# Optimization experiments

Hardware: AMD Instinct MI355X
Metric: run time of the kernel (lower is better)

The kernel has to match this reference:

```python
import jax, jax.numpy as jnp
import numpy as np

N_NODES = 100000


def _gcn_layer(x, W, b, row, col, norm, n_nodes):
    # x: [N, Fin], W: [Fin, Fout]. GCN: A_hat @ (x W) + b with symmetric norm.
    xw = x @ W                                   # [N, Fout]
    msg = xw[row] * norm[:, None]                # [E+N, Fout] gathered messages
    agg = jax.ops.segment_sum(msg, col, num_segments=n_nodes)  # scatter-add at dst
    return agg + b


def setup_inputs() -> dict:
    key = jax.random.key(0)
    ks = jax.random.split(key, 5)
    N, E = N_NODES, 1600000
    Fin, F1, F2, C = 512, 64, 128, 40
    x = jax.random.normal(ks[0], (N, Fin), dtype=jnp.float32)
    edge_index = jax.random.randint(ks[1], (2, E), 0, N, dtype=jnp.int64)
    W1 = jax.random.normal(ks[2], (Fin, F1), dtype=jnp.float32) / np.sqrt(Fin)
    W2 = jax.random.normal(ks[3], (F1, F2), dtype=jnp.float32) / np.sqrt(F1)
    W3 = jax.random.normal(ks[4], (F2, C), dtype=jnp.float32) / np.sqrt(F2)
    return {
        "x": x, "edge_index": edge_index,
        "W1": W1, "b1": jnp.zeros((F1,), jnp.float32),
        "W2": W2, "b2": jnp.zeros((F2,), jnp.float32),
        "W3": W3, "b3": jnp.zeros((C,), jnp.float32),
    }


def reference(x, edge_index, W1, b1, W2, b2, W3, b3):
    N = x.shape[0]
    # Add self-loops (GCNConv default add_self_loops=True)
    loop = jnp.arange(N, dtype=edge_index.dtype)
    row = jnp.concatenate([edge_index[0], loop])  # source nodes
    col = jnp.concatenate([edge_index[1], loop])  # destination nodes
    # Symmetric degree normalization: deg computed at destination with self-loops
    deg = jax.ops.segment_sum(jnp.ones_like(col, dtype=x.dtype), col, num_segments=N)
    dis = jax.lax.rsqrt(deg)                      # deg >= 1 due to self-loops
    norm = dis[row] * dis[col]                    # [E+N]

    h1 = jax.nn.relu(_gcn_layer(x, W1, b1, row, col, norm, N))
    # dropout is identity (training=False)
    h2 = jax.nn.relu(_gcn_layer(h1, W2, b2, row, col, norm, N))
    h3 = _gcn_layer(h2, W3, b3, row, col, norm, N)
    return jax.nn.log_softmax(h3, axis=1)
```

## Files before the change

kernel.cpp:

```cpp
#include <hip/hip_runtime.h>
#include <math.h>


typedef __attribute__((ext_vector_type(8))) short short8;
typedef __attribute__((ext_vector_type(4))) float f32x4;

__device__ __forceinline__ unsigned short f2bf(float f) {
    unsigned int u = __float_as_uint(f);
    unsigned int r = (u + 0x7fffu + ((u >> 16) & 1u)) >> 16;
    return (unsigned short)r;
}
__device__ __forceinline__ float bflo(unsigned int u) { return __uint_as_float(u << 16); }
__device__ __forceinline__ float bfhi(unsigned int u) { return __uint_as_float(u & 0xffff0000u); }

__device__ __forceinline__ void wprep_one(const float* W, unsigned short* out,
                                          int KS, int FOUT, int t) {
    int i = t & 7;
    int l = (t >> 3) & 63;
    int g = t >> 9;
    int ks = g % KS;
    int nt = g / KS;
    int k = ks * 32 + (l >> 4) * 8 + i;
    int c = nt * 16 + (l & 15);
    out[t] = (c < FOUT) ? f2bf(W[(size_t)k * FOUT + c]) : (unsigned short)0;
}

__global__ void prep_kernel(const float* __restrict__ W1, const float* __restrict__ W2,
                            const float* __restrict__ W3,
                            unsigned short* __restrict__ Wf1, unsigned short* __restrict__ Wf2,
                            unsigned short* __restrict__ Wf3,
                            int* __restrict__ cnt, int* __restrict__ fillc, int N) {
    int t = blockIdx.x * 256 + threadIdx.x;
    if (t < 32768)       wprep_one(W1, Wf1, 16, 64, t);
    else if (t < 40960)  wprep_one(W2, Wf2, 2, 128, t - 32768);
    else if (t < 47104)  wprep_one(W3, Wf3, 4, 40, t - 40960);
    if (t < N) cnt[t] = 0;
    else if (t < 2 * N) fillc[t - N] = 0;
}

__global__ void count_kernel(const int* __restrict__ col, int* __restrict__ cnt, int E) {
    int e = blockIdx.x * 256 + threadIdx.x;
    if (e < E) atomicAdd(&cnt[col[e]], 1);
}

__global__ void scan1_kernel(const int* __restrict__ cnt, int* __restrict__ out,
                             int* __restrict__ bsums, int n) {
    __shared__ int s[1024];
    int i = blockIdx.x * 1024 + threadIdx.x;
    int v = (i < n) ? cnt[i] : 0;
    s[threadIdx.x] = v;
    __syncthreads();
    for (int off = 1; off < 1024; off <<= 1) {
        int t = 0;
        if ((int)threadIdx.x >= off) t = s[threadIdx.x - off];
        __syncthreads();
        if ((int)threadIdx.x >= off) s[threadIdx.x] += t;
        __syncthreads();
    }
    if (i < n) out[i] = s[threadIdx.x] - v;
    if (threadIdx.x == 1023) bsums[blockIdx.x] = s[1023];
}

__global__ void scan2_kernel(int* bsums, int nb) {
    __shared__ int s[128];
    int v = ((int)threadIdx.x < nb) ? bsums[threadIdx.x] : 0;
    s[threadIdx.x] = v;
    __syncthreads();
    for (int off = 1; off < 128; off <<= 1) {
        int t = 0;
        if ((int)threadIdx.x >= off) t = s[threadIdx.x - off];
        __syncthreads();
        if ((int)threadIdx.x >= off) s[threadIdx.x] += t;
        __syncthreads();
    }
    if ((int)threadIdx.x < nb) bsums[threadIdx.x] = s[threadIdx.x] - v;
}

__global__ void scan3d_kernel(int* __restrict__ ptr, const int* __restrict__ bsums,
                              const int* __restrict__ cnt, float* __restrict__ dis,
                              int n, int E) {
    int i = blockIdx.x * 1024 + threadIdx.x;
    if (i < n) {
        ptr[i] += bsums[blockIdx.x];
        dis[i] = rsqrtf((float)(cnt[i] + 1));
    }
    if (i == 0) ptr[n] = E;
}

__global__ void fill_kernel(const int* __restrict__ row, const int* __restrict__ col,
                            const int* __restrict__ ptr, int* __restrict__ fillc,
                            const float* __restrict__ dis, uint2* __restrict__ csr_en, int E) {
    int e = blockIdx.x * 256 + threadIdx.x;
    if (e < E) {
        int c = col[e];
        int r = row[e];
        int p = ptr[c] + atomicAdd(&fillc[c], 1);
        uint2 en;
        en.x = (unsigned int)r;
        en.y = __float_as_uint(dis[r] * dis[c]);
        csr_en[p] = en;
    }
}

__global__ __launch_bounds__(256) void gemm1_kernel(const float* __restrict__ Ap,
                                                    const unsigned short* __restrict__ Wf,
                                                    unsigned short* __restrict__ Y, int N) {
    __shared__ unsigned short As[2][64][136];
    const int t = threadIdx.x;
    const int lane = t & 63;
    const int wid = t >> 6;
    const int rbase = blockIdx.x * 64;
    const int fr = lane & 15;
    const int khalf = lane >> 4;

    f32x4 acc[4];
#pragma unroll
    for (int nt = 0; nt < 4; nt++)
#pragma unroll
        for (int j = 0; j < 4; j++) acc[nt][j] = 0.f;

    auto stage = [&](int buf, int c) {
#pragma unroll
        for (int rd = 0; rd < 8; rd++) {
            int u = t + rd * 256;
            int row = u >> 5;
            int q = u & 31;
            int gr = rbase + row; if (gr > N - 1) gr = N - 1;
            float4 v = *(const float4*)(Ap + (size_t)gr * 512 + c * 128 + q * 4);
            uint2 w;
            w.x = (unsigned int)f2bf(v.x) | ((unsigned int)f2bf(v.y) << 16);
            w.y = (unsigned int)f2bf(v.z) | ((unsigned int)f2bf(v.w) << 16);
            *(uint2*)&As[buf][row][q * 4] = w;
        }
    };

    stage(0, 0);
    __syncthreads();
#pragma unroll
    for (int c = 0; c < 4; c++) {
        if (c < 3) stage((c + 1) & 1, c + 1);
#pragma unroll
        for (int ks = 0; ks < 4; ks++) {
            short8 afr = *(const short8*)&As[c & 1][wid * 16 + fr][ks * 32 + khalf * 8];
            const int ksg = c * 4 + ks;
#pragma unroll
            for (int nt = 0; nt < 4; nt++) {
                short8 bfr = *(const short8*)(Wf + (((size_t)nt * 16 + ksg) * 64 + lane) * 8);
                acc[nt] = __builtin_amdgcn_mfma_f32_16x16x32_bf16(afr, bfr, acc[nt], 0, 0, 0);
            }
        }
        __syncthreads();
    }

    const int rD0 = rbase + wid * 16 + (lane >> 4) * 4;
    const int colb = lane & 15;
#pragma unroll
    for (int nt = 0; nt < 4; nt++) {
        int c = nt * 16 + colb;
#pragma unroll
        for (int i = 0; i < 4; i++) {
            int rD = rD0 + i;
            if (rD < N) Y[(size_t)rD * 64 + c] = f2bf(acc[nt][i]);
        }
    }
}

__global__ __launch_bounds__(256) void gemm23_kernel(const unsigned short* __restrict__ A,
                                                     const unsigned short* __restrict__ Wf2,
                                                     const float* __restrict__ b2,
                                                     const unsigned short* __restrict__ Wf3,
                                                     unsigned short* __restrict__ Y, int N) {
    __shared__ unsigned short hs[4][16][136];
    const int lane = threadIdx.x & 63;
    const int wid = threadIdx.x >> 6;
    const int rbase = blockIdx.x * 64 + wid * 16;
    const int rA = rbase + (lane & 15);
    const bool va = rA < N;
    const int khalf = lane >> 4;

    f32x4 acc2[8];
#pragma unroll
    for (int nt = 0; nt < 8; nt++)
#pragma unroll
        for (int j = 0; j < 4; j++) acc2[nt][j] = 0.f;

#pragma unroll
    for (int ks = 0; ks < 2; ks++) {
        short8 afr;
        if (va) afr = *(const short8*)(A + (size_t)rA * 64 + ks * 32 + khalf * 8);
        else {
#pragma unroll
            for (int j = 0; j < 8; j++) afr[j] = 0;
        }
#pragma unroll
        for (int nt = 0; nt < 8; nt++) {
            short8 bfr = *(const short8*)(Wf2 + (((size_t)nt * 2 + ks) * 64 + lane) * 8);
            acc2[nt] = __builtin_amdgcn_mfma_f32_16x16x32_bf16(afr, bfr, acc2[nt], 0, 0, 0);
        }
    }

    const int rD = (lane >> 4) * 4;
    const int colb = lane & 15;
#pragma unroll
    for (int nt = 0; nt < 8; nt++) {
        int c = nt * 16 + colb;
        float bv = b2[c];
#pragma unroll
        for (int j = 0; j < 4; j++)
            hs[wid][rD + j][c] = f2bf(fmaxf(acc2[nt][j] + bv, 0.f));
    }
    __syncthreads();

    f32x4 acc3[3];
#pragma unroll
    for (int nt = 0; nt < 3; nt++)
#pragma unroll
        for (int j = 0; j < 4; j++) acc3[nt][j] = 0.f;

    const int r = lane & 15;
#pragma unroll
    for (int ks = 0; ks < 4; ks++) {
        short8 afr = *(const short8*)&hs[wid][r][ks * 32 + khalf * 8];
#pragma unroll
        for (int nt = 0; nt < 3; nt++) {
            short8 bfr = *(const short8*)(Wf3 + (((size_t)nt * 4 + ks) * 64 + lane) * 8);
            acc3[nt] = __builtin_amdgcn_mfma_f32_16x16x32_bf16(afr, bfr, acc3[nt], 0, 0, 0);
        }
    }

#pragma unroll
    for (int nt = 0; nt < 3; nt++) {
        int c = nt * 16 + colb;
        if (c < 40) {
#pragma unroll
            for (int i = 0; i < 4; i++) {
                int rr = rbase + rD + i;
                if (rr < N) Y[(size_t)rr * 40 + c] = f2bf(acc3[nt][i]);
            }
        }
    }
}

template <bool BR>
__global__ __launch_bounds__(256) void agg64_kernel(const unsigned int* __restrict__ XW,
                                                    const float* __restrict__ bias,
                                                    const int* __restrict__ ptr,
                                                    const uint2* __restrict__ EN,
                                                    unsigned int* __restrict__ Y, int N) {
    const int lane = threadIdx.x & 63;
    const int wid = threadIdx.x >> 6;
    const int n = blockIdx.x * 4 + wid;
    if (n >= N) return;
    const int s = lane >> 3;
    const int q = lane & 7;

    const int e0 = ptr[n], e1 = ptr[n + 1];
    const float selfw = 1.0f / (float)(e1 - e0 + 1);

    float acc[8];
    if (s == 0) {
        const uint4 u = *(const uint4*)(XW + (size_t)n * 32 + q * 4);
        acc[0] = selfw * bflo(u.x); acc[1] = selfw * bfhi(u.x);
        acc[2] = selfw * bflo(u.y); acc[3] = selfw * bfhi(u.y);
        acc[4] = selfw * bflo(u.z); acc[5] = selfw * bfhi(u.z);
        acc[6] = selfw * bflo(u.w); acc[7] = selfw * bfhi(u.w);
    } else {
#pragma unroll
        for (int j = 0; j < 8; j++) acc[j] = 0.f;
    }

    for (int eb = e0; eb < e1; eb += 64) {
        int cnt = e1 - eb; if (cnt > 64) cnt = 64;
        uint2 en;
        if (lane < cnt) en = EN[eb + lane];
        else { en.x = 0; en.y = 0; }
#pragma unroll 2
        for (int k = s; k < cnt; k += 8) {
            int r = __shfl((int)en.x, k);
            float nrm = __uint_as_float((unsigned int)__shfl((int)en.y, k));
            const uint4 u = *(const uint4*)(XW + (size_t)r * 32 + q * 4);
            acc[0] += nrm * bflo(u.x); acc[1] += nrm * bfhi(u.x);
            acc[2] += nrm * bflo(u.y); acc[3] += nrm * bfhi(u.y);
            acc[4] += nrm * bflo(u.z); acc[5] += nrm * bfhi(u.z);
            acc[6] += nrm * bflo(u.w); acc[7] += nrm * bfhi(u.w);
        }
    }

#pragma unroll
    for (int off = 8; off < 64; off <<= 1)
#pragma unroll
        for (int j = 0; j < 8; j++) acc[j] += __shfl_xor(acc[j], off);

    if (lane < 8) {
        float v[8];
        if (BR) {
            const float4 b0 = *((const float4*)bias + lane * 2);
            const float4 b1 = *((const float4*)bias + lane * 2 + 1);
            v[0] = fmaxf(acc[0] + b0.x, 0.f); v[1] = fmaxf(acc[1] + b0.y, 0.f);
            v[2] = fmaxf(acc[2] + b0.z, 0.f); v[3] = fmaxf(acc[3] + b0.w, 0.f);
            v[4] = fmaxf(acc[4] + b1.x, 0.f); v[5] = fmaxf(acc[5] + b1.y, 0.f);
            v[6] = fmaxf(acc[6] + b1.z, 0.f); v[7] = fmaxf(acc[7] + b1.w, 0.f);
        } else {
#pragma unroll
            for (int j = 0; j < 8; j++) v[j] = acc[j];
        }
        uint4 o;
        o.x = (unsigned int)f2bf(v[0]) | ((unsigned int)f2bf(v[1]) << 16);
        o.y = (unsigned int)f2bf(v[2]) | ((unsigned int)f2bf(v[3]) << 16);
        o.z = (unsigned int)f2bf(v[4]) | ((unsigned int)f2bf(v[5]) << 16);
        o.w = (unsigned int)f2bf(v[6]) | ((unsigned int)f2bf(v[7]) << 16);
        *(uint4*)(Y + (size_t)n * 32 + lane * 4) = o;
    }
}

__global__ __launch_bounds__(256) void agg40lsm_kernel(const unsigned int* __restrict__ XW,
                                                       const float* __restrict__ bias,
                                                       const int* __restrict__ ptr,
                                                       const uint2* __restrict__ EN,
                                                       float* __restrict__ out, int N) {
    const int lane = threadIdx.x & 63;
    const int wid = threadIdx.x >> 6;
    const int n = blockIdx.x * 4 + wid;
    if (n >= N) return;
    const int s = lane >> 4;
    const int c = lane & 15;
    const bool act = (c < 10);

    const int e0 = ptr[n], e1 = ptr[n + 1];
    const float selfw = 1.0f / (float)(e1 - e0 + 1);

    float acc[4] = {0.f, 0.f, 0.f, 0.f};
    if (s == 0 && act) {
        const uint2 u = *(const uint2*)(XW + (size_t)n * 20 + c * 2);
        acc[0] = selfw * bflo(u.x); acc[1] = selfw * bfhi(u.x);
        acc[2] = selfw * bflo(u.y); acc[3] = selfw * bfhi(u.y);
    }

    for (int eb = e0; eb < e1; eb += 64) {
        int cnt = e1 - eb; if (cnt > 64) cnt = 64;
        uint2 en;
        if (lane < cnt) en = EN[eb + lane];
        else { en.x = 0; en.y = 0; }
#pragma unroll 2
        for (int k = s; k < cnt; k += 4) {
            int r = __shfl((int)en.x, k);
            float nrm = __uint_as_float((unsigned int)__shfl((int)en.y, k));
            if (act) {
                const uint2 u = *(const uint2*)(XW + (size_t)r * 20 + c * 2);
                acc[0] += nrm * bflo(u.x); acc[1] += nrm * bfhi(u.x);
                acc[2] += nrm * bflo(u.y); acc[3] += nrm * bfhi(u.y);
            }
        }
    }

#pragma unroll
    for (int off = 16; off < 64; off <<= 1)
#pragma unroll
        for (int j = 0; j < 4; j++) acc[j] += __shfl_xor(acc[j], off);

    float v[4];
    float m = -INFINITY;
    if (lane < 16 && act) {
        const float4 b = *((const float4*)bias + c);
        v[0] = acc[0] + b.x; v[1] = acc[1] + b.y;
        v[2] = acc[2] + b.z; v[3] = acc[3] + b.w;
        m = fmaxf(fmaxf(v[0], v[1]), fmaxf(v[2], v[3]));
    }
#pragma unroll
    for (int off = 32; off; off >>= 1) m = fmaxf(m, __shfl_xor(m, off));
    float ex = 0.f;
    if (lane < 16 && act)
        ex = expf(v[0] - m) + expf(v[1] - m) + expf(v[2] - m) + expf(v[3] - m);
#pragma unroll
    for (int off = 32; off; off >>= 1) ex += __shfl_xor(ex, off);
    float ls = logf(ex);
    if (lane < 16 && act) {
        float4 o;
        o.x = v[0] - m - ls; o.y = v[1] - m - ls;
        o.z = v[2] - m - ls; o.w = v[3] - m - ls;
        *(float4*)(out + (size_t)n * 40 + c * 4) = o;
    }
}


extern "C" void kernel_launch(void* const* d_in, const int* in_sizes, int n_in,
                              void* d_out, int out_size, void* d_ws, size_t ws_size,
                              hipStream_t stream) {
    const float* x  = (const float*)d_in[0];
    const int*   ei = (const int*)d_in[1];
    const float* W1 = (const float*)d_in[2];
    const float* b1 = (const float*)d_in[3];
    const float* W2 = (const float*)d_in[4];
    const float* b2 = (const float*)d_in[5];
    const float* W3 = (const float*)d_in[6];
    const float* b3 = (const float*)d_in[7];
    const int N = in_sizes[0] / 512;
    const int E = in_sizes[1] / 2;
    const int* row = ei;
    const int* col = ei + E;

    char* p = (char*)d_ws;
    auto alloc = [&](size_t bytes) {
        void* r = (void*)p;
        p += (bytes + 255) & ~(size_t)255;
        return r;
    };
    float* dis    = (float*)alloc((size_t)N * 4);
    int*   cnt    = (int*)alloc((size_t)N * 4);
    int*   ptr    = (int*)alloc((size_t)(N + 1) * 4);
    int*   fillc  = (int*)alloc((size_t)N * 4);
    int*   bsums  = (int*)alloc(1024);
    uint2* csr_en = (uint2*)alloc((size_t)E * 8);
    unsigned short* Wf1 = (unsigned short*)alloc(4 * 16 * 64 * 8 * 2);
    unsigned short* Wf2 = (unsigned short*)alloc(8 * 2 * 64 * 8 * 2);
    unsigned short* Wf3 = (unsigned short*)alloc(3 * 4 * 64 * 8 * 2);
    unsigned short* xw1 = (unsigned short*)alloc((size_t)N * 64 * 2);
    unsigned short* h1  = (unsigned short*)alloc((size_t)N * 64 * 2);
    unsigned short* a2  = (unsigned short*)alloc((size_t)N * 64 * 2);
    unsigned short* xw3 = (unsigned short*)alloc((size_t)N * 40 * 2);
    float* out = (float*)d_out;

    prep_kernel<<<(2 * N + 255) / 256, 256, 0, stream>>>(W1, W2, W3, Wf1, Wf2, Wf3,
                                                         cnt, fillc, N);

    const int cgrid = (E + 255) / 256;
    count_kernel<<<cgrid, 256, 0, stream>>>(col, cnt, E);

    const int ggrid = (N + 63) / 64;
    gemm1_kernel<<<ggrid, 256, 0, stream>>>(x, Wf1, xw1, N);

    int nb = (N + 1023) / 1024;
    scan1_kernel<<<nb, 1024, 0, stream>>>(cnt, ptr, bsums, N);
    scan2_kernel<<<1, 128, 0, stream>>>(bsums, nb);
    scan3d_kernel<<<nb, 1024, 0, stream>>>(ptr, bsums, cnt, dis, N, E);
    fill_kernel<<<cgrid, 256, 0, stream>>>(row, col, ptr, fillc, dis, csr_en, E);

    const int ngrid = (N + 3) / 4;

    agg64_kernel<true><<<ngrid, 256, 0, stream>>>((const unsigned int*)xw1, b1, ptr, csr_en,
                                                  (unsigned int*)h1, N);
    agg64_kernel<false><<<ngrid, 256, 0, stream>>>((const unsigned int*)h1, nullptr, ptr, csr_en,
                                                   (unsigned int*)a2, N);
    gemm23_kernel<<<ggrid, 256, 0, stream>>>(a2, Wf2, b2, Wf3, xw3, N);
    agg40lsm_kernel<<<ngrid, 256, 0, stream>>>((const unsigned int*)xw3, b3, ptr, csr_en, out, N);
}
```

Measured before the change: 364.9 us.

## Record CSR slots during counting and process two nodes per wave in agg64

The count kernel now saves each edge's atomic return value as its slot within the destination bucket. The fill kernel then places edges without a second atomic pass or a zeroed fill counter, at the cost of an extra E-sized int buffer written and read. The 64-feature aggregation kernel now has each wavefront handle two destination nodes, interleaving their gathers so more memory loads are in flight per wave. This also halves the grid size, raises register use, and adds divergence when the two nodes' degrees differ.

```diff
diff --git a/kernel.cpp b/kernel.cpp
--- a/kernel.cpp
+++ b/kernel.cpp
@@ -29,18 +29,18 @@
                             const float* __restrict__ W3,
                             unsigned short* __restrict__ Wf1, unsigned short* __restrict__ Wf2,
                             unsigned short* __restrict__ Wf3,
-                            int* __restrict__ cnt, int* __restrict__ fillc, int N) {
+                            int* __restrict__ cnt, int N) {
     int t = blockIdx.x * 256 + threadIdx.x;
     if (t < 32768)       wprep_one(W1, Wf1, 16, 64, t);
     else if (t < 40960)  wprep_one(W2, Wf2, 2, 128, t - 32768);
     else if (t < 47104)  wprep_one(W3, Wf3, 4, 40, t - 40960);
     if (t < N) cnt[t] = 0;
-    else if (t < 2 * N) fillc[t - N] = 0;
-}
-
-__global__ void count_kernel(const int* __restrict__ col, int* __restrict__ cnt, int E) {
+}
+
+__global__ void countslot_kernel(const int* __restrict__ col, int* __restrict__ cnt,
+                                 int* __restrict__ slot, int E) {
     int e = blockIdx.x * 256 + threadIdx.x;
-    if (e < E) atomicAdd(&cnt[col[e]], 1);
+    if (e < E) slot[e] = atomicAdd(&cnt[col[e]], 1);
 }
 
 __global__ void scan1_kernel(const int* __restrict__ cnt, int* __restrict__ out,
@@ -88,13 +88,13 @@
 }
 
 __global__ void fill_kernel(const int* __restrict__ row, const int* __restrict__ col,
-                            const int* __restrict__ ptr, int* __restrict__ fillc,
+                            const int* __restrict__ ptr, const int* __restrict__ slot,
                             const float* __restrict__ dis, uint2* __restrict__ csr_en, int E) {
     int e = blockIdx.x * 256 + threadIdx.x;
     if (e < E) {
         int c = col[e];
         int r = row[e];
-        int p = ptr[c] + atomicAdd(&fillc[c], 1);
+        int p = ptr[c] + slot[e];
         uint2 en;
         en.x = (unsigned int)r;
         en.y = __float_as_uint(dis[r] * dis[c]);
@@ -249,67 +249,104 @@
                                                     unsigned int* __restrict__ Y, int N) {
     const int lane = threadIdx.x & 63;
     const int wid = threadIdx.x >> 6;
-    const int n = blockIdx.x * 4 + wid;
-    if (n >= N) return;
+    const int nA = (blockIdx.x * 4 + wid) * 2;
+    const int nB = nA + 1;
+    if (nA >= N) return;
+    const bool hasB = (nB < N);
     const int s = lane >> 3;
     const int q = lane & 7;
 
-    const int e0 = ptr[n], e1 = ptr[n + 1];
-    const float selfw = 1.0f / (float)(e1 - e0 + 1);
-
-    float acc[8];
+    const int e0A = ptr[nA], e1A = ptr[nA + 1];
+    const int e0B = hasB ? ptr[nB] : 0;
+    const int e1B = hasB ? ptr[nB + 1] : 0;
+    const float selfwA = 1.0f / (float)(e1A - e0A + 1);
+    const float selfwB = hasB ? 1.0f / (float)(e1B - e0B + 1) : 0.f;
+
+    float accA[8], accB[8];
+#pragma unroll
+    for (int j = 0; j < 8; j++) { accA[j] = 0.f; accB[j] = 0.f; }
     if (s == 0) {
-        const uint4 u = *(const uint4*)(XW + (size_t)n * 32 + q * 4);
-        acc[0] = selfw * bflo(u.x); acc[1] = selfw * bfhi(u.x);
-        acc[2] = selfw * bflo(u.y); acc[3] = selfw * bfhi(u.y);
-        acc[4] = selfw * bflo(u.z); acc[5] = selfw * bfhi(u.z);
-        acc[6] = selfw * bflo(u.w); acc[7] = selfw * bfhi(u.w);
-    } else {
-#pragma unroll
-        for (int j = 0; j < 8; j++) acc[j] = 0.f;
-    }
-
-    for (int eb = e0; eb < e1; eb += 64) {
-        int cnt = e1 - eb; if (cnt > 64) cnt = 64;
-        uint2 en;
-        if (lane < cnt) en = EN[eb + lane];
-        else { en.x = 0; en.y = 0; }
-#pragma unroll 2
-        for (int k = s; k < cnt; k += 8) {
-            int r = __shfl((int)en.x, k);
-            float nrm = __uint_as_float((unsigned int)__shfl((int)en.y, k));
-            const uint4 u = *(const uint4*)(XW + (size_t)r * 32 + q * 4);
-            acc[0] += nrm * bflo(u.x); acc[1] += nrm * bfhi(u.x);
-            acc[2] += nrm * bflo(u.y); acc[3] += nrm * bfhi(u.y);
-            acc[4] += nrm * bflo(u.z); acc[5] += nrm * bfhi(u.z);
-            acc[6] += nrm * bflo(u.w); acc[7] += nrm * bfhi(u.w);
+        const uint4 uA = *(const uint4*)(XW + (size_t)nA * 32 + q * 4);
+        accA[0] = selfwA * bflo(uA.x); accA[1] = selfwA * bfhi(uA.x);
+        accA[2] = selfwA * bflo(uA.y); accA[3] = selfwA * bfhi(uA.y);
+        accA[4] = selfwA * bflo(uA.z); accA[5] = selfwA * bfhi(uA.z);
+        accA[6] = selfwA * bflo(uA.w); accA[7] = selfwA * bfhi(uA.w);
+        if (hasB) {
+            const uint4 uB = *(const uint4*)(XW + (size_t)nB * 32 + q * 4);
+            accB[0] = selfwB * bflo(uB.x); accB[1] = selfwB * bfhi(uB.x);
+            accB[2] = selfwB * bflo(uB.y); accB[3] = selfwB * bfhi(uB.y);
+            accB[4] = selfwB * bflo(uB.z); accB[5] = selfwB * bfhi(uB.z);
+            accB[6] = selfwB * bflo(uB.w); accB[7] = selfwB * bfhi(uB.w);
+        }
+    }
+
+    for (int ebA = e0A, ebB = e0B; ebA < e1A || ebB < e1B; ebA += 64, ebB += 64) {
+        int cntA = e1A - ebA; if (cntA > 64) cntA = 64; if (cntA < 0) cntA = 0;
+        int cntB = e1B - ebB; if (cntB > 64) cntB = 64; if (cntB < 0) cntB = 0;
+        uint2 enA, enB;
+        if (lane < cntA) enA = EN[ebA + lane]; else { enA.x = 0; enA.y = 0; }
+        if (lane < cntB) enB = EN[ebB + lane]; else { enB.x = 0; enB.y = 0; }
+        int kmax = cntA > cntB ? cntA : cntB;
+        for (int k = s; k < kmax; k += 8) {
+            if (k < cntA) {
+                int r = __shfl((int)enA.x, k);
+                float nrm = __uint_as_float((unsigned int)__shfl((int)enA.y, k));
+                const uint4 u = *(const uint4*)(XW + (size_t)r * 32 + q * 4);
+                accA[0] += nrm * bflo(u.x); accA[1] += nrm * bfhi(u.x);
+                accA[2] += nrm * bflo(u.y); accA[3] += nrm * bfhi(u.y);
+                accA[4] += nrm * bflo(u.z); accA[5] += nrm * bfhi(u.z);
+                accA[6] += nrm * bflo(u.w); accA[7] += nrm * bfhi(u.w);
+            }
+            if (k < cntB) {
+                int r = __shfl((int)enB.x, k);
+                float nrm = __uint_as_float((unsigned int)__shfl((int)enB.y, k));
+                const uint4 u = *(const uint4*)(XW + (size_t)r * 32 + q * 4);
+                accB[0] += nrm * bflo(u.x); accB[1] += nrm * bfhi(u.x);
+                accB[2] += nrm * bflo(u.y); accB[3] += nrm * bfhi(u.y);
+                accB[4] += nrm * bflo(u.z); accB[5] += nrm * bfhi(u.z);
+                accB[6] += nrm * bflo(u.w); accB[7] += nrm * bfhi(u.w);
+            }
         }
     }
 
 #pragma unroll
     for (int off = 8; off < 64; off <<= 1)
 #pragma unroll
-        for (int j = 0; j < 8; j++) acc[j] += __shfl_xor(acc[j], off);
+        for (int j = 0; j < 8; j++) {
+            accA[j] += __shfl_xor(accA[j], off);
+            accB[j] += __shfl_xor(accB[j], off);
+        }
 
     if (lane < 8) {
-        float v[8];
+        float vA[8], vB[8];
         if (BR) {
             const float4 b0 = *((const float4*)bias + lane * 2);
             const float4 b1 = *((const float4*)bias + lane * 2 + 1);
-            v[0] = fmaxf(acc[0] + b0.x, 0.f); v[1] = fmaxf(acc[1] + b0.y, 0.f);
-            v[2] = fmaxf(acc[2] + b0.z, 0.f); v[3] = fmaxf(acc[3] + b0.w, 0.f);
-            v[4] = fmaxf(acc[4] + b1.x, 0.f); v[5] = fmaxf(acc[5] + b1.y, 0.f);
-            v[6] = fmaxf(acc[6] + b1.z, 0.f); v[7] = fmaxf(acc[7] + b1.w, 0.f);
+            vA[0] = fmaxf(accA[0] + b0.x, 0.f); vA[1] = fmaxf(accA[1] + b0.y, 0.f);
+            vA[2] = fmaxf(accA[2] + b0.z, 0.f); vA[3] = fmaxf(accA[3] + b0.w, 0.f);
+            vA[4] = fmaxf(accA[4] + b1.x, 0.f); vA[5] = fmaxf(accA[5] + b1.y, 0.f);
+            vA[6] = fmaxf(accA[6] + b1.z, 0.f); vA[7] = fmaxf(accA[7] + b1.w, 0.f);
+            vB[0] = fmaxf(accB[0] + b0.x, 0.f); vB[1] = fmaxf(accB[1] + b0.y, 0.f);
+            vB[2] = fmaxf(accB[2] + b0.z, 0.f); vB[3] = fmaxf(accB[3] + b0.w, 0.f);
+            vB[4] = fmaxf(accB[4] + b1.x, 0.f); vB[5] = fmaxf(accB[5] + b1.y, 0.f);
+            vB[6] = fmaxf(accB[6] + b1.z, 0.f); vB[7] = fmaxf(accB[7] + b1.w, 0.f);
         } else {
 #pragma unroll
-            for (int j = 0; j < 8; j++) v[j] = acc[j];
-        }
-        uint4 o;
-        o.x = (unsigned int)f2bf(v[0]) | ((unsigned int)f2bf(v[1]) << 16);
-        o.y = (unsigned int)f2bf(v[2]) | ((unsigned int)f2bf(v[3]) << 16);
-        o.z = (unsigned int)f2bf(v[4]) | ((unsigned int)f2bf(v[5]) << 16);
-        o.w = (unsigned int)f2bf(v[6]) | ((unsigned int)f2bf(v[7]) << 16);
-        *(uint4*)(Y + (size_t)n * 32 + lane * 4) = o;
+            for (int j = 0; j < 8; j++) { vA[j] = accA[j]; vB[j] = accB[j]; }
+        }
+        uint4 oA, oB;
+        oA.x = (unsigned int)f2bf(vA[0]) | ((unsigned int)f2bf(vA[1]) << 16);
+        oA.y = (unsigned int)f2bf(vA[2]) | ((unsigned int)f2bf(vA[3]) << 16);
+        oA.z = (unsigned int)f2bf(vA[4]) | ((unsigned int)f2bf(vA[5]) << 16);
+        oA.w = (unsigned int)f2bf(vA[6]) | ((unsigned int)f2bf(vA[7]) << 16);
+        *(uint4*)(Y + (size_t)nA * 32 + lane * 4) = oA;
+        if (hasB) {
+            oB.x = (unsigned int)f2bf(vB[0]) | ((unsigned int)f2bf(vB[1]) << 16);
+            oB.y = (unsigned int)f2bf(vB[2]) | ((unsigned int)f2bf(vB[3]) << 16);
+            oB.z = (unsigned int)f2bf(vB[4]) | ((unsigned int)f2bf(vB[5]) << 16);
+            oB.w = (unsigned int)f2bf(vB[6]) | ((unsigned int)f2bf(vB[7]) << 16);
+            *(uint4*)(Y + (size_t)nB * 32 + lane * 4) = oB;
+        }
     }
 }
 
@@ -408,7 +445,7 @@
     float* dis    = (float*)alloc((size_t)N * 4);
     int*   cnt    = (int*)alloc((size_t)N * 4);
     int*   ptr    = (int*)alloc((size_t)(N + 1) * 4);
-    int*   fillc  = (int*)alloc((size_t)N * 4);
+    int*   slot   = (int*)alloc((size_t)E * 4);
     int*   bsums  = (int*)alloc(1024);
     uint2* csr_en = (uint2*)alloc((size_t)E * 8);
     unsigned short* Wf1 = (unsigned short*)alloc(4 * 16 * 64 * 8 * 2);
@@ -420,11 +457,10 @@
     unsigned short* xw3 = (unsigned short*)alloc((size_t)N * 40 * 2);
     float* out = (float*)d_out;
 
-    prep_kernel<<<(2 * N + 255) / 256, 256, 0, stream>>>(W1, W2, W3, Wf1, Wf2, Wf3,
-                                                         cnt, fillc, N);
+    prep_kernel<<<(2 * N + 255) / 256, 256, 0, stream>>>(W1, W2, W3, Wf1, Wf2, Wf3, cnt, N);
 
     const int cgrid = (E + 255) / 256;
-    count_kernel<<<cgrid, 256, 0, stream>>>(col, cnt, E);
+    countslot_kernel<<<cgrid, 256, 0, stream>>>(col, cnt, slot, E);
 
     const int ggrid = (N + 63) / 64;
     gemm1_kernel<<<ggrid, 256, 0, stream>>>(x, Wf1, xw1, N);
@@ -433,14 +469,15 @@
     scan1_kernel<<<nb, 1024, 0, stream>>>(cnt, ptr, bsums, N);
     scan2_kernel<<<1, 128, 0, stream>>>(bsums, nb);
     scan3d_kernel<<<nb, 1024, 0, stream>>>(ptr, bsums, cnt, dis, N, E);
-    fill_kernel<<<cgrid, 256, 0, stream>>>(row, col, ptr, fillc, dis, csr_en, E);
-
-    const int ngrid = (N + 3) / 4;
-
-    agg64_kernel<true><<<ngrid, 256, 0, stream>>>((const unsigned int*)xw1, b1, ptr, csr_en,
-                                                  (unsigned int*)h1, N);
-    agg64_kernel<false><<<ngrid, 256, 0, stream>>>((const unsigned int*)h1, nullptr, ptr, csr_en,
-                                                   (unsigned int*)a2, N);
+    fill_kernel<<<cgrid, 256, 0, stream>>>(row, col, ptr, slot, dis, csr_en, E);
+
+    const int ngrid2 = (N + 7) / 8;
+    const int ngrid  = (N + 3) / 4;
+
+    agg64_kernel<true><<<ngrid2, 256, 0, stream>>>((const unsigned int*)xw1, b1, ptr, csr_en,
+                                                   (unsigned int*)h1, N);
+    agg64_kernel<false><<<ngrid2, 256, 0, stream>>>((const unsigned int*)h1, nullptr, ptr, csr_en,
+                                                    (unsigned int*)a2, N);
     gemm23_kernel<<<ggrid, 256, 0, stream>>>(a2, Wf2, b2, Wf3, xw3, N);
     agg40lsm_kernel<<<ngrid, 256, 0, stream>>>((const unsigned int*)xw3, b3, ptr, csr_en, out, N);
 }
```

After: 330.9 us. -9.3%, faster.
